# Kernel optimization log

Measured on AMD Instinct MI355X. Metric: run time of the kernel, lower is better.

Reference implementation:

```python
import jax, jax.numpy as jnp
import numpy as np

B, S, E, H = 4, 2048, 1024, 16
D = E // H  # head_dim = 64
SCALE = D ** -0.5
THETA = 10000.0


def _rope_tables(seq_len, head_dim):
    half = head_dim // 2
    inv_freq = 1.0 / (THETA ** (jnp.arange(half, dtype=jnp.float32) / half))
    ang = jnp.arange(seq_len, dtype=jnp.float32)[:, None] * inv_freq[None, :]  # [S, D/2]
    ang = jnp.concatenate([ang, ang], axis=-1)  # [S, D]
    return jnp.cos(ang), jnp.sin(ang)


def setup_inputs() -> dict:
    key = jax.random.key(0)
    kx, kw, ko = jax.random.split(key, 3)
    x = jax.random.normal(kx, (B, S, E), dtype=jnp.float32)
    in_proj_weight = jax.random.normal(kw, (3 * E, E), dtype=jnp.float32) * (E ** -0.5)
    in_proj_bias = jnp.zeros((3 * E,), dtype=jnp.float32)
    out_w = jax.random.normal(ko, (E, E), dtype=jnp.float32) * (E ** -0.5)
    out_b = jnp.zeros((E,), dtype=jnp.float32)
    cos, sin = _rope_tables(S, D)
    return {"x": x, "in_proj_weight": in_proj_weight, "in_proj_bias": in_proj_bias,
            "out_w": out_w, "out_b": out_b, "cos": cos, "sin": sin}


def _rotate_half(t):
    t1, t2 = jnp.split(t, 2, axis=-1)
    return jnp.concatenate([-t2, t1], axis=-1)


def reference(x, in_proj_weight, in_proj_bias, out_w, out_b, cos, sin):
    b, s, e = x.shape
    # fused QKV projection: [b, s, 3E]
    proj = x @ in_proj_weight.T + in_proj_bias
    q, k, v = jnp.split(proj, 3, axis=-1)
    # b s (h d) -> b h s d
    to_heads = lambda t: t.reshape(b, s, H, D).transpose(0, 2, 1, 3)
    q, k, v = to_heads(q), to_heads(k), to_heads(v)
    # RoPE (rotate-half) on q, k; cos/sin: [S, D] broadcast over batch/heads
    c = cos[None, None, :, :]
    sn = sin[None, None, :, :]
    q = q * c + _rotate_half(q) * sn
    k = k * c + _rotate_half(k) * sn
    # SDPA, non-causal, explicit scale = head_dim**-0.5
    scores = jnp.einsum("bhqd,bhkd->bhqk", q, k) * SCALE
    attn = jax.nn.softmax(scores, axis=-1)
    o = jnp.einsum("bhqk,bhkd->bhqd", attn, v)
    # b h s d -> b s (h d)
    o = o.transpose(0, 2, 1, 3).reshape(b, s, e)
    return o @ out_w.T + out_b
```

## Files before the change

### kernel.cpp

```cpp
#include <hip/hip_runtime.h>

#define NB 4
#define NS 2048
#define NE 1024
#define NH 16
#define ND 64
#define KVB 64

typedef unsigned short ushort_t;
typedef __attribute__((ext_vector_type(8))) short bf16x8;
typedef __attribute__((ext_vector_type(4))) float f32x4;

#define SCALE_LOG2E 0.18033688011112042f

static __device__ __forceinline__ ushort_t f2bf(float f) {
    union { float f; unsigned int u; } v; v.f = f;
    unsigned int r = v.u + 0x7FFF + ((v.u >> 16) & 1);
    return (ushort_t)(r >> 16);
}

static __device__ __forceinline__ unsigned pk_bf16(float lo, float hi) {
    unsigned r;
    asm("v_cvt_pk_bf16_f32 %0, %1, %2" : "=v"(r) : "v"(lo), "v"(hi));
    return r;
}

static __device__ __forceinline__ void gload16(const void* g, void* l) {
    __builtin_amdgcn_global_load_lds(
        (const __attribute__((address_space(1))) void*)g,
        (__attribute__((address_space(3))) void*)l,
        16, 0, 0);
}

__global__ __launch_bounds__(256)
void cvt_f32_bf16(const float* __restrict__ src, ushort_t* __restrict__ dst, int n8)
{
    const int i = blockIdx.x * 256 + threadIdx.x;
    if (i >= n8) return;
    const float4 a = ((const float4*)src)[i * 2];
    const float4 b = ((const float4*)src)[i * 2 + 1];
    union { ushort_t us[8]; uint4 v; } pk;
    pk.us[0] = f2bf(a.x); pk.us[1] = f2bf(a.y); pk.us[2] = f2bf(a.z); pk.us[3] = f2bf(a.w);
    pk.us[4] = f2bf(b.x); pk.us[5] = f2bf(b.y); pk.us[6] = f2bf(b.z); pk.us[7] = f2bf(b.w);
    ((uint4*)dst)[i] = pk.v;
}

template<int EPI>
__global__ __launch_bounds__(256)
void gemm_bf16(const ushort_t* __restrict__ A, const ushort_t* __restrict__ W,
               const float* __restrict__ bias, float* __restrict__ C,
               ushort_t* __restrict__ Cb, int M, int N, int K)
{
    __shared__ ushort_t As[128 * 32];
    __shared__ ushort_t Bs[128 * 32];
    const int tid  = threadIdx.x;
    const int lane = tid & 63;
    const int wid  = tid >> 6;
    const int lr   = lane & 15;
    const int lg   = lane >> 4;
    const int m0 = blockIdx.y * 128;
    const int n0 = blockIdx.x * 128;
    const int wr = wid >> 1, wc = wid & 1;

    size_t srcoff[2];
    int ldsoff[2];
#pragma unroll
    for (int p = 0; p < 2; ++p) {
        const int chunk = p * 256 + tid;
        const int row = chunk >> 2;
        const int sp  = chunk & 3;
        const int c   = sp ^ ((row >> 1) & 3);
        srcoff[p] = (size_t)row * K + c * 8;
        ldsoff[p] = (p * 256 + wid * 64) * 8;
    }
    const ushort_t* Ag = A + (size_t)m0 * K;
    const ushort_t* Wg = W + (size_t)n0 * K;

    int offa[4], offb[4];
#pragma unroll
    for (int f = 0; f < 4; ++f) {
        const int ra = wr * 64 + f * 16 + lr;
        offa[f] = ra * 32 + (lg ^ ((ra >> 1) & 3)) * 8;
        const int rb = wc * 64 + f * 16 + lr;
        offb[f] = rb * 32 + (lg ^ ((rb >> 1) & 3)) * 8;
    }

    f32x4 acc[4][4];
#pragma unroll
    for (int i = 0; i < 4; ++i)
#pragma unroll
        for (int j = 0; j < 4; ++j) acc[i][j] = (f32x4){0.f, 0.f, 0.f, 0.f};

    for (int k0 = 0; k0 < K; k0 += 32) {
        __syncthreads();
#pragma unroll
        for (int p = 0; p < 2; ++p) {
            gload16(Ag + srcoff[p] + k0, (ushort_t*)As + ldsoff[p]);
            gload16(Wg + srcoff[p] + k0, (ushort_t*)Bs + ldsoff[p]);
        }
        __syncthreads();
        bf16x8 af[4], bfr[4];
#pragma unroll
        for (int f = 0; f < 4; ++f) {
            af[f]  = *(const bf16x8*)&As[offa[f]];
            bfr[f] = *(const bf16x8*)&Bs[offb[f]];
        }
#pragma unroll
        for (int mf = 0; mf < 4; ++mf)
#pragma unroll
            for (int nf = 0; nf < 4; ++nf)
                acc[mf][nf] = __builtin_amdgcn_mfma_f32_16x16x32_bf16(
                    af[mf], bfr[nf], acc[mf][nf], 0, 0, 0);
    }

    if (EPI == 0) {
#pragma unroll
        for (int nf = 0; nf < 4; ++nf) {
            const int n = n0 + wc * 64 + nf * 16 + lr;
            const float bj = bias[n];
#pragma unroll
            for (int mf = 0; mf < 4; ++mf)
#pragma unroll
                for (int r = 0; r < 4; ++r) {
                    const int m = m0 + wr * 64 + mf * 16 + lg * 4 + r;
                    C[(size_t)m * N + n] = acc[mf][nf][r] + bj;
                }
        }
    } else {
#pragma unroll
        for (int nf = 0; nf < 4; ++nf) {
            const int n = n0 + wc * 64 + nf * 16 + lr;
            const float bj = bias[n];
            const int t = n >> 10;
            const int h = (n >> 6) & (NH - 1);
            const int d = n & (ND - 1);
#pragma unroll
            for (int mf = 0; mf < 4; ++mf)
#pragma unroll
                for (int r = 0; r < 4; ++r) {
                    const int m = m0 + wr * 64 + mf * 16 + lg * 4 + r;
                    const int b = m >> 11;
                    const int s = m & (NS - 1);
                    Cb[((size_t)((t * NB + b) * NH + h) * NS + s) * ND + d] =
                        f2bf(acc[mf][nf][r] + bj);
                }
        }
    }
}

__global__ __launch_bounds__(256)
void rope_bf16(ushort_t* __restrict__ qkvb, const float* __restrict__ cosT,
               const float* __restrict__ sinT)
{
    const int idx = blockIdx.x * 256 + threadIdx.x;
    const int d0 = (idx & 3) * 8;
    const int s  = (idx >> 2) & (NS - 1);
    const int h  = (idx >> 13) & (NH - 1);
    const int b  = (idx >> 17) & (NB - 1);
    const int t  = idx >> 19;
    ushort_t* base = qkvb + ((size_t)((t * NB + b) * NH + h) * NS + s) * ND;

    union { ushort_t us[8]; uint4 v; } lo, hi, loo, hio;
    lo.v = *(const uint4*)(base + d0);
    hi.v = *(const uint4*)(base + d0 + 32);
    const float4 c0 = *(const float4*)(cosT + s * ND + d0);
    const float4 c1 = *(const float4*)(cosT + s * ND + d0 + 4);
    const float4 s0 = *(const float4*)(sinT + s * ND + d0);
    const float4 s1 = *(const float4*)(sinT + s * ND + d0 + 4);
    const float cc[8] = {c0.x, c0.y, c0.z, c0.w, c1.x, c1.y, c1.z, c1.w};
    const float ss[8] = {s0.x, s0.y, s0.z, s0.w, s1.x, s1.y, s1.z, s1.w};
#pragma unroll
    for (int j = 0; j < 8; ++j) {
        union { unsigned u; float f; } a, bb;
        a.u  = ((unsigned)lo.us[j]) << 16;
        bb.u = ((unsigned)hi.us[j]) << 16;
        loo.us[j] = f2bf(a.f * cc[j] - bb.f * ss[j]);
        hio.us[j] = f2bf(bb.f * cc[j] + a.f * ss[j]);
    }
    *(uint4*)(base + d0)      = loo.v;
    *(uint4*)(base + d0 + 32) = hio.v;
}

__global__ __launch_bounds__(256)
void attn_kernel(const ushort_t* __restrict__ qkvb, ushort_t* __restrict__ obuf)
{
    __shared__ ushort_t Ks[64 * 72];
    __shared__ ushort_t Vs[64 * 64];
    __shared__ ushort_t Ps[128 * 72];

    const int tid  = threadIdx.x;
    const int lane = tid & 63;
    const int wid  = tid >> 6;
    const int lr   = lane & 15;
    const int lg   = lane >> 4;

    const int orig = blockIdx.x;
    const int wg   = (orig & 7) * 128 + (orig >> 3);
    const int bh   = wg >> 4;
    const int b = bh >> 4, h = bh & (NH - 1);
    const int q0 = (wg & 15) * 128;

    const ushort_t* qbase = qkvb + ((size_t)((0 * NB + b) * NH + h)) * (NS * ND);
    const ushort_t* kbase = qkvb + ((size_t)((1 * NB + b) * NH + h)) * (NS * ND);
    const ushort_t* vbase = qkvb + ((size_t)((2 * NB + b) * NH + h)) * (NS * ND);

    bf16x8 qf[2][2];
#pragma unroll
    for (int st = 0; st < 2; ++st)
#pragma unroll
        for (int kh = 0; kh < 2; ++kh)
            qf[st][kh] = *(const bf16x8*)(qbase + (size_t)(q0 + wid * 32 + st * 16 + lr) * ND
                                          + kh * 32 + lg * 8);

    const int sc = tid & 7;
    const int sr0 = tid >> 3;

    uint4 krg[2], vrg[2];
#pragma unroll
    for (int it = 0; it < 2; ++it) {
        const int r = sr0 + it * 32;
        krg[it] = *(const uint4*)(kbase + r * ND + sc * 8);
        vrg[it] = *(const uint4*)(vbase + r * ND + sc * 8);
    }

    f32x4 acc_o[2][4];
    float lsum[2] = {0.f, 0.f};
#pragma unroll
    for (int st = 0; st < 2; ++st)
#pragma unroll
        for (int dk = 0; dk < 4; ++dk) acc_o[st][dk] = (f32x4){0.f, 0.f, 0.f, 0.f};

    for (int kt = 0; kt < NS; kt += KVB) {
        __syncthreads();
#pragma unroll
        for (int it = 0; it < 2; ++it) {
            const int r = sr0 + it * 32;
            *(uint4*)&Ks[r * 72 + sc * 8] = krg[it];
            union { uint4 v; ushort_t us[8]; } pu;
            pu.v = vrg[it];
#pragma unroll
            for (int j = 0; j < 8; ++j) {
                const int sw = (j ^ sc) << 4;
                Vs[(sc * 8 + j) * 64 + ((((r * 2) ^ sw)) >> 1)] = pu.us[j];
            }
        }
        __syncthreads();
        if (kt + KVB < NS) {
#pragma unroll
            for (int it = 0; it < 2; ++it) {
                const int r = kt + KVB + sr0 + it * 32;
                krg[it] = *(const uint4*)(kbase + (size_t)r * ND + sc * 8);
                vrg[it] = *(const uint4*)(vbase + (size_t)r * ND + sc * 8);
            }
        }

        f32x4 s[2][4];
#pragma unroll
        for (int st = 0; st < 2; ++st)
#pragma unroll
            for (int kvf = 0; kvf < 4; ++kvf) s[st][kvf] = (f32x4){0.f, 0.f, 0.f, 0.f};
        __builtin_amdgcn_s_setprio(1);
#pragma unroll
        for (int kh = 0; kh < 2; ++kh)
#pragma unroll
            for (int kvf = 0; kvf < 4; ++kvf) {
                const bf16x8 kf = *(const bf16x8*)&Ks[(kvf * 16 + lr) * 72 + kh * 32 + lg * 8];
                s[0][kvf] = __builtin_amdgcn_mfma_f32_16x16x32_bf16(kf, qf[0][kh], s[0][kvf], 0, 0, 0);
                s[1][kvf] = __builtin_amdgcn_mfma_f32_16x16x32_bf16(kf, qf[1][kh], s[1][kvf], 0, 0, 0);
            }
        __builtin_amdgcn_s_setprio(0);

#pragma unroll
        for (int st = 0; st < 2; ++st) {
            const int prow = (wid * 32 + st * 16 + lr) * 72;
#pragma unroll
            for (int kvf = 0; kvf < 4; ++kvf) {
                const float p0 = __builtin_amdgcn_exp2f(s[st][kvf][0] * SCALE_LOG2E);
                const float p1 = __builtin_amdgcn_exp2f(s[st][kvf][1] * SCALE_LOG2E);
                const float p2 = __builtin_amdgcn_exp2f(s[st][kvf][2] * SCALE_LOG2E);
                const float p3 = __builtin_amdgcn_exp2f(s[st][kvf][3] * SCALE_LOG2E);
                lsum[st] += (p0 + p1) + (p2 + p3);
                const unsigned w01 = pk_bf16(p0, p1);
                const unsigned w23 = pk_bf16(p2, p3);
                *(uint2*)&Ps[prow + kvf * 16 + lg * 4] = make_uint2(w01, w23);
            }
        }
        __syncthreads();

        __builtin_amdgcn_s_setprio(1);
#pragma unroll
        for (int kh = 0; kh < 2; ++kh) {
            const bf16x8 pf0 = *(const bf16x8*)&Ps[(wid * 32 + 0  + lr) * 72 + kh * 32 + lg * 8];
            const bf16x8 pf1 = *(const bf16x8*)&Ps[(wid * 32 + 16 + lr) * 72 + kh * 32 + lg * 8];
#pragma unroll
            for (int dk = 0; dk < 4; ++dk) {
                const int d = dk * 16 + lr;
                const int sw = ((d & 7) ^ ((d >> 3) & 7)) << 4;
                const bf16x8 vf = *(const bf16x8*)&Vs[d * 64 + (((kh * 64 + lg * 16) ^ sw) >> 1)];
                acc_o[0][dk] = __builtin_amdgcn_mfma_f32_16x16x32_bf16(pf0, vf, acc_o[0][dk], 0, 0, 0);
                acc_o[1][dk] = __builtin_amdgcn_mfma_f32_16x16x32_bf16(pf1, vf, acc_o[1][dk], 0, 0, 0);
            }
        }
        __builtin_amdgcn_s_setprio(0);
    }

#pragma unroll
    for (int st = 0; st < 2; ++st) {
        float r = lsum[st];
        r += __shfl_xor(r, 16);
        r += __shfl_xor(r, 32);
        float invq[4];
#pragma unroll
        for (int reg = 0; reg < 4; ++reg)
            invq[reg] = 1.0f / __shfl(r, lg * 4 + reg);
#pragma unroll
        for (int dk = 0; dk < 4; ++dk)
#pragma unroll
            for (int reg = 0; reg < 4; ++reg) {
                const int q = q0 + wid * 32 + st * 16 + lg * 4 + reg;
                const int d = dk * 16 + lr;
                obuf[((size_t)(b * NS + q)) * NE + h * ND + d] =
                    f2bf(acc_o[st][dk][reg] * invq[reg]);
            }
    }
}

extern "C" void kernel_launch(void* const* d_in, const int* in_sizes, int n_in,
                              void* d_out, int out_size, void* d_ws, size_t ws_size,
                              hipStream_t stream)
{
    const float* x    = (const float*)d_in[0];
    const float* Win  = (const float*)d_in[1];
    const float* bin  = (const float*)d_in[2];
    const float* Wout = (const float*)d_in[3];
    const float* bout = (const float*)d_in[4];
    const float* cosT = (const float*)d_in[5];
    const float* sinT = (const float*)d_in[6];
    float* out  = (float*)d_out;

    ushort_t* qkvb  = (ushort_t*)d_ws;
    ushort_t* obufb = qkvb + (size_t)3 * NB * NH * NS * ND;
    ushort_t* xb    = obufb + (size_t)NB * NS * NE;
    ushort_t* Wib   = xb + (size_t)NB * NS * NE;
    ushort_t* Wob   = Wib + (size_t)3 * NE * NE;

    const int nx = NB * NS * NE;
    const int nwi = 3 * NE * NE;
    const int nwo = NE * NE;

    cvt_f32_bf16<<<nx / 2048, 256, 0, stream>>>(x, xb, nx / 8);
    cvt_f32_bf16<<<nwi / 2048, 256, 0, stream>>>(Win, Wib, nwi / 8);
    cvt_f32_bf16<<<nwo / 2048, 256, 0, stream>>>(Wout, Wob, nwo / 8);

    gemm_bf16<1><<<dim3(3 * NE / 128, NB * NS / 128), 256, 0, stream>>>(
        xb, Wib, bin, nullptr, qkvb, NB * NS, 3 * NE, NE);
    rope_bf16<<<(2 * NB * NH * NS * 4) / 256, 256, 0, stream>>>(qkvb, cosT, sinT);
    attn_kernel<<<dim3(NB * NH * (NS / 128)), 256, 0, stream>>>(qkvb, obufb);
    gemm_bf16<0><<<dim3(NE / 128, NB * NS / 128), 256, 0, stream>>>(
        obufb, Wob, bout, out, nullptr, NB * NS, NE, NE);
}
```

Before: 258.7 us.

## Store V transposed from QKV GEMM and load K/V fragments directly from global

The QKV projection epilogue now writes V in a transposed [b,h,d,s] layout, so attention can load V fragments as contiguous 16-byte reads straight from global memory. Attention drops the shared-memory K and V tiles and their block-wide barriers. Each wave loads its K and V MFMA fragments directly from global (L2), and the P-tile barrier becomes a wave-local lgkmcnt wait, since each wave only reads its own P rows. This removes LDS staging and syncs, but adds redundant global/L2 traffic because all four waves reload the same K/V, and loses the register prefetch pipelining. The transposed V store from the GEMM is also strided by NS, which makes those writes poorly coalesced.

Result: slower. 375.5 us (+45.1%).

```diff
diff --git a/kernel.cpp b/kernel.cpp
--- a/kernel.cpp
+++ b/kernel.cpp
@@ -127,24 +127,38 @@
                 }
         }
     } else {
+        const int tt = n0 >> 10;
+        float bj[4]; int hh[4];
 #pragma unroll
         for (int nf = 0; nf < 4; ++nf) {
             const int n = n0 + wc * 64 + nf * 16 + lr;
-            const float bj = bias[n];
-            const int t = n >> 10;
-            const int h = (n >> 6) & (NH - 1);
-            const int d = n & (ND - 1);
-#pragma unroll
-            for (int mf = 0; mf < 4; ++mf)
-#pragma unroll
-                for (int r = 0; r < 4; ++r) {
-                    const int m = m0 + wr * 64 + mf * 16 + lg * 4 + r;
-                    const int b = m >> 11;
-                    const int s = m & (NS - 1);
-                    Cb[((size_t)((t * NB + b) * NH + h) * NS + s) * ND + d] =
-                        f2bf(acc[mf][nf][r] + bj);
+            bj[nf] = bias[n];
+            hh[nf] = (n >> 6) & (NH - 1);
+        }
+        const size_t vtoff = (size_t)2 * NB * NH * NS * ND;
+#pragma unroll
+        for (int mf = 0; mf < 4; ++mf)
+#pragma unroll
+            for (int r = 0; r < 4; ++r) {
+                const int m = m0 + wr * 64 + mf * 16 + lg * 4 + r;
+                const int b = m >> 11;
+                const int s = m & (NS - 1);
+                if (tt == 2) {
+#pragma unroll
+                    for (int nf = 0; nf < 4; ++nf) {
+                        const int d = nf * 16 + lr;
+                        Cb[vtoff + ((size_t)(b * NH + hh[nf]) * ND + d) * NS + s] =
+                            f2bf(acc[mf][nf][r] + bj[nf]);
+                    }
+                } else {
+#pragma unroll
+                    for (int nf = 0; nf < 4; ++nf) {
+                        const int d = nf * 16 + lr;
+                        Cb[((size_t)((tt * NB + b) * NH + hh[nf]) * NS + s) * ND + d] =
+                            f2bf(acc[mf][nf][r] + bj[nf]);
+                    }
                 }
-        }
+            }
     }
 }
 
@@ -184,8 +198,6 @@
 __global__ __launch_bounds__(256)
 void attn_kernel(const ushort_t* __restrict__ qkvb, ushort_t* __restrict__ obuf)
 {
-    __shared__ ushort_t Ks[64 * 72];
-    __shared__ ushort_t Vs[64 * 64];
     __shared__ ushort_t Ps[128 * 72];
 
     const int tid  = threadIdx.x;
@@ -200,9 +212,10 @@
     const int b = bh >> 4, h = bh & (NH - 1);
     const int q0 = (wg & 15) * 128;
 
-    const ushort_t* qbase = qkvb + ((size_t)((0 * NB + b) * NH + h)) * (NS * ND);
-    const ushort_t* kbase = qkvb + ((size_t)((1 * NB + b) * NH + h)) * (NS * ND);
-    const ushort_t* vbase = qkvb + ((size_t)((2 * NB + b) * NH + h)) * (NS * ND);
+    const ushort_t* qbase  = qkvb + ((size_t)((0 * NB + b) * NH + h)) * (NS * ND);
+    const ushort_t* kbase  = qkvb + ((size_t)((1 * NB + b) * NH + h)) * (NS * ND);
+    const ushort_t* vtbase = qkvb + (size_t)2 * NB * NH * NS * ND
+                                  + (size_t)(b * NH + h) * ND * NS;
 
     bf16x8 qf[2][2];
 #pragma unroll
@@ -212,17 +225,6 @@
             qf[st][kh] = *(const bf16x8*)(qbase + (size_t)(q0 + wid * 32 + st * 16 + lr) * ND
                                           + kh * 32 + lg * 8);
 
-    const int sc = tid & 7;
-    const int sr0 = tid >> 3;
-
-    uint4 krg[2], vrg[2];
-#pragma unroll
-    for (int it = 0; it < 2; ++it) {
-        const int r = sr0 + it * 32;
-        krg[it] = *(const uint4*)(kbase + r * ND + sc * 8);
-        vrg[it] = *(const uint4*)(vbase + r * ND + sc * 8);
-    }
-
     f32x4 acc_o[2][4];
     float lsum[2] = {0.f, 0.f};
 #pragma unroll
@@ -231,28 +233,13 @@
         for (int dk = 0; dk < 4; ++dk) acc_o[st][dk] = (f32x4){0.f, 0.f, 0.f, 0.f};
 
     for (int kt = 0; kt < NS; kt += KVB) {
-        __syncthreads();
-#pragma unroll
-        for (int it = 0; it < 2; ++it) {
-            const int r = sr0 + it * 32;
-            *(uint4*)&Ks[r * 72 + sc * 8] = krg[it];
-            union { uint4 v; ushort_t us[8]; } pu;
-            pu.v = vrg[it];
-#pragma unroll
-            for (int j = 0; j < 8; ++j) {
-                const int sw = (j ^ sc) << 4;
-                Vs[(sc * 8 + j) * 64 + ((((r * 2) ^ sw)) >> 1)] = pu.us[j];
-            }
-        }
-        __syncthreads();
-        if (kt + KVB < NS) {
-#pragma unroll
-            for (int it = 0; it < 2; ++it) {
-                const int r = kt + KVB + sr0 + it * 32;
-                krg[it] = *(const uint4*)(kbase + (size_t)r * ND + sc * 8);
-                vrg[it] = *(const uint4*)(vbase + (size_t)r * ND + sc * 8);
-            }
-        }
+        bf16x8 kf[2][4];
+#pragma unroll
+        for (int kh = 0; kh < 2; ++kh)
+#pragma unroll
+            for (int kvf = 0; kvf < 4; ++kvf)
+                kf[kh][kvf] = *(const bf16x8*)(kbase
+                    + (size_t)(kt + kvf * 16 + lr) * ND + kh * 32 + lg * 8);
 
         f32x4 s[2][4];
 #pragma unroll
@@ -264,11 +251,18 @@
         for (int kh = 0; kh < 2; ++kh)
 #pragma unroll
             for (int kvf = 0; kvf < 4; ++kvf) {
-                const bf16x8 kf = *(const bf16x8*)&Ks[(kvf * 16 + lr) * 72 + kh * 32 + lg * 8];
-                s[0][kvf] = __builtin_amdgcn_mfma_f32_16x16x32_bf16(kf, qf[0][kh], s[0][kvf], 0, 0, 0);
-                s[1][kvf] = __builtin_amdgcn_mfma_f32_16x16x32_bf16(kf, qf[1][kh], s[1][kvf], 0, 0, 0);
+                s[0][kvf] = __builtin_amdgcn_mfma_f32_16x16x32_bf16(kf[kh][kvf], qf[0][kh], s[0][kvf], 0, 0, 0);
+                s[1][kvf] = __builtin_amdgcn_mfma_f32_16x16x32_bf16(kf[kh][kvf], qf[1][kh], s[1][kvf], 0, 0, 0);
             }
         __builtin_amdgcn_s_setprio(0);
+
+        bf16x8 vf[2][4];
+#pragma unroll
+        for (int kh = 0; kh < 2; ++kh)
+#pragma unroll
+            for (int dk = 0; dk < 4; ++dk)
+                vf[kh][dk] = *(const bf16x8*)(vtbase
+                    + (size_t)(dk * 16 + lr) * NS + kt + kh * 32 + lg * 8);
 
 #pragma unroll
         for (int st = 0; st < 2; ++st) {
@@ -285,7 +279,8 @@
                 *(uint2*)&Ps[prow + kvf * 16 + lg * 4] = make_uint2(w01, w23);
             }
         }
-        __syncthreads();
+        asm volatile("s_waitcnt lgkmcnt(0)" ::: "memory");
+        __builtin_amdgcn_sched_barrier(0);
 
         __builtin_amdgcn_s_setprio(1);
 #pragma unroll
@@ -294,11 +289,8 @@
             const bf16x8 pf1 = *(const bf16x8*)&Ps[(wid * 32 + 16 + lr) * 72 + kh * 32 + lg * 8];
 #pragma unroll
             for (int dk = 0; dk < 4; ++dk) {
-                const int d = dk * 16 + lr;
-                const int sw = ((d & 7) ^ ((d >> 3) & 7)) << 4;
-                const bf16x8 vf = *(const bf16x8*)&Vs[d * 64 + (((kh * 64 + lg * 16) ^ sw) >> 1)];
-                acc_o[0][dk] = __builtin_amdgcn_mfma_f32_16x16x32_bf16(pf0, vf, acc_o[0][dk], 0, 0, 0);
-                acc_o[1][dk] = __builtin_amdgcn_mfma_f32_16x16x32_bf16(pf1, vf, acc_o[1][dk], 0, 0, 0);
+                acc_o[0][dk] = __builtin_amdgcn_mfma_f32_16x16x32_bf16(pf0, vf[kh][dk], acc_o[0][dk], 0, 0, 0);
+                acc_o[1][dk] = __builtin_amdgcn_mfma_f32_16x16x32_bf16(pf1, vf[kh][dk], acc_o[1][dk], 0, 0, 0);
             }
         }
         __builtin_amdgcn_s_setprio(0);
```
